# Kernel optimization log

Measured on AMD Instinct MI355X. Metric: run time of the kernel, lower is better.

## Reference

```python
import jax, jax.numpy as jnp
import numpy as np

N_NODES = 100000
N_EDGES = 1600000
N_FEAT = 128
HIDDEN = 128
N_CLASSES = 40
MAX_DEPTH = 4
INIT_TEMP = 1.0  # temperature (non-trainable)
N_AGGR = 3       # ['mean', 'max', 'self']


def setup_inputs() -> dict:
    key = jax.random.key(0)
    ks = jax.random.split(key, 16)
    s = 1.0 / np.sqrt(HIDDEN)
    inp = {
        'x': jax.random.normal(ks[0], (N_NODES, N_FEAT), dtype=jnp.float32),
        'edge_index': jax.random.randint(ks[1], (2, N_EDGES), 0, N_NODES, dtype=jnp.int32),
        'W_pre': jax.random.normal(ks[2], (N_FEAT, HIDDEN), dtype=jnp.float32) / np.sqrt(N_FEAT),
        'b_pre': jnp.zeros((HIDDEN,), dtype=jnp.float32),
        'W_depth': jax.random.normal(ks[3], (HIDDEN, 2), dtype=jnp.float32) * s,
        'b_depth': jnp.zeros((2,), dtype=jnp.float32),
        'W_aggr': jax.random.normal(ks[4], (HIDDEN, N_AGGR), dtype=jnp.float32) * s,
        'b_aggr': jnp.zeros((N_AGGR,), dtype=jnp.float32),
        'W_conv': jax.random.normal(ks[5], (MAX_DEPTH, HIDDEN, HIDDEN), dtype=jnp.float32) * s,
        'b_conv': jnp.zeros((MAX_DEPTH, HIDDEN), dtype=jnp.float32),
        'W_post': jax.random.normal(ks[6], (HIDDEN, N_CLASSES), dtype=jnp.float32) * s,
        'b_post': jnp.zeros((N_CLASSES,), dtype=jnp.float32),
    }
    return inp


def _mix_aggr_conv(x, src, dst, deg, W, b, aggr_w):
    # MixAggrConvLayer: transform then per-node convex mix of {mean, max, self}
    h = x @ W + b                                   # [N, H]
    msg = h[src]                                    # [E, H] gather
    mean_a = jax.ops.segment_sum(msg, dst, num_segments=N_NODES) / deg[:, None]
    max_a = jax.ops.segment_max(msg, dst, num_segments=N_NODES)
    max_a = jnp.where(jnp.isfinite(max_a), max_a, 0.0)  # isolated nodes -> 0
    return aggr_w[:, 0:1] * mean_a + aggr_w[:, 1:2] * max_a + aggr_w[:, 2:3] * h


def reference(x, edge_index, W_pre, b_pre, W_depth, b_depth, W_aggr, b_aggr,
              W_conv, b_conv, W_post, b_post):
    src, dst = edge_index[0], edge_index[1]
    deg = jnp.maximum(
        jax.ops.segment_sum(jnp.ones((src.shape[0],), jnp.float32), dst,
                            num_segments=N_NODES), 1.0)

    # pre_mp + (Dropout eval = identity) + ReLU
    h = jax.nn.relu(x @ W_pre + b_pre)              # [N, H]

    continue_pr = jnp.ones((N_NODES,), jnp.float32)
    selected = jnp.zeros((N_NODES, HIDDEN), jnp.float32)
    for i in range(MAX_DEPTH):
        hd = jax.lax.stop_gradient(h)               # controllers see detached x
        stop_prob = jax.nn.softmax((hd @ W_depth + b_depth) / INIT_TEMP, axis=-1)
        aggr_prob = jax.nn.softmax((hd @ W_aggr + b_aggr) / INIT_TEMP, axis=-1)
        h = _mix_aggr_conv(h, src, dst, deg, W_conv[i], b_conv[i], aggr_prob)
        h = jax.nn.relu(h)                          # dropout (eval) + relu
        selected = selected + (continue_pr * stop_prob[:, 1])[:, None] * h
        continue_pr = continue_pr * stop_prob[:, 0]

    logits = selected @ W_post + b_post             # [N, C]
    return jax.nn.log_softmax(logits, axis=1)
```

## Files before the change

kernel.cpp:

```cpp
#include <hip/hip_runtime.h>
#include <math.h>

#define HIDDEN 128
#define NCLS 40
#define BMAX 1024

typedef __attribute__((ext_vector_type(8))) short short8;
typedef __attribute__((ext_vector_type(4))) float f32x4;
typedef __attribute__((ext_vector_type(2))) float f32x2;

__device__ __forceinline__ unsigned short f2bf(float f) {
    unsigned u = __float_as_uint(f);
    unsigned r = u + 0x7FFFu + ((u >> 16) & 1u);
    return (unsigned short)(r >> 16);
}
__device__ __forceinline__ float bf_lo(unsigned u) { return __uint_as_float(u << 16); }
__device__ __forceinline__ float bf_hi(unsigned u) { return __uint_as_float(u & 0xFFFF0000u); }

__global__ void k_wprep(const float* __restrict__ Wp, const float* __restrict__ Wc,
                        const float* __restrict__ Wd, const float* __restrict__ Wa,
                        unsigned short* __restrict__ WpreT, unsigned short* __restrict__ WT) {
    int i = blockIdx.x * 256 + threadIdx.x;
    if (i < 16384) {
        int n = i >> 7, k = i & 127;
        WpreT[i] = f2bf(Wp[k * 128 + n]);
    } else if (i < 16384 + 4 * 18432) {
        int j = i - 16384;
        int d = j / 18432;
        int rem = j % 18432;
        int n = rem >> 7, k = rem & 127;
        float v = 0.f;
        if (n < 128)      v = Wc[d * 16384 + k * 128 + n];
        else if (n < 130) v = Wd[k * 2 + (n - 128)];
        else if (n < 133) v = Wa[k * 3 + (n - 130)];
        WT[j] = f2bf(v);
    }
}


__launch_bounds__(256)
__global__ void k_bcount(const int* __restrict__ ei, int E, int* __restrict__ bucket_cnt) {
    __shared__ int hist[BMAX];
    const int tid = threadIdx.x;
    for (int i = tid; i < BMAX; i += 256) hist[i] = 0;
    __syncthreads();
    const int e0 = blockIdx.x * 4096;
    #pragma unroll
    for (int i = 0; i < 16; i++) {
        int e = e0 + i * 256 + tid;
        if (e < E) atomicAdd(&hist[ei[E + e] >> 8], 1);
    }
    __syncthreads();
    for (int i = tid; i < BMAX; i += 256) {
        int v = hist[i];
        if (v > 0) atomicAdd(&bucket_cnt[i], v);
    }
}

__global__ void k_bscan(const int* __restrict__ bucket_cnt, int nb,
                        int* __restrict__ bucket_base, int* __restrict__ bucket_cursor) {
    __shared__ int sd[256];
    const int tid = threadIdx.x;
    int v[4];
    int sum = 0;
    #pragma unroll
    for (int j = 0; j < 4; j++) {
        int b = tid * 4 + j;
        v[j] = (b < nb) ? bucket_cnt[b] : 0;
        sum += v[j];
    }
    sd[tid] = sum;
    __syncthreads();
    #pragma unroll
    for (int off = 1; off < 256; off <<= 1) {
        int t = (tid >= off) ? sd[tid - off] : 0;
        __syncthreads();
        sd[tid] += t;
        __syncthreads();
    }
    int base = sd[tid] - sum;
    #pragma unroll
    for (int j = 0; j < 4; j++) {
        int b = tid * 4 + j;
        if (b < nb) {
            bucket_base[b] = base;
            bucket_cursor[b] = base;
            base += v[j];
        }
    }
}

__launch_bounds__(256)
__global__ void k_bin(const int* __restrict__ ei, int E,
                      int* __restrict__ bucket_cursor, unsigned* __restrict__ binned) {
    __shared__ int hist[BMAX];
    __shared__ int rankc[BMAX];
    __shared__ int lbase[BMAX];
    const int tid = threadIdx.x;
    const int e0 = blockIdx.x * 4096;
    for (int i = tid; i < BMAX; i += 256) { hist[i] = 0; rankc[i] = 0; }
    __syncthreads();
    int bkt[16];
    unsigned pk[16];
    #pragma unroll
    for (int i = 0; i < 16; i++) {
        int e = e0 + i * 256 + tid;
        if (e < E) {
            int s = ei[e];
            int d = ei[E + e];
            bkt[i] = d >> 8;
            pk[i] = ((unsigned)(d & 255) << 24) | (unsigned)s;
            atomicAdd(&hist[bkt[i]], 1);
        } else bkt[i] = -1;
    }
    __syncthreads();
    for (int i = tid; i < BMAX; i += 256)
        if (hist[i] > 0) lbase[i] = atomicAdd(&bucket_cursor[i], hist[i]);
    __syncthreads();
    #pragma unroll
    for (int i = 0; i < 16; i++) {
        if (bkt[i] >= 0) {
            int r = atomicAdd(&rankc[bkt[i]], 1);
            binned[lbase[bkt[i]] + r] = pk[i];
        }
    }
}

__launch_bounds__(256)
__global__ void k_scatter(const unsigned* __restrict__ binned,
                          const int* __restrict__ bucket_base,
                          const int* __restrict__ bucket_cnt,
                          int* __restrict__ row_start, int* __restrict__ deg_i,
                          float* __restrict__ degf,
                          int* __restrict__ csr_off, int N) {
    __shared__ int hist[256];
    __shared__ int rs[256];
    __shared__ int cur[256];
    const int tid = threadIdx.x;
    hist[tid] = 0;
    __syncthreads();
    const int base = bucket_base[blockIdx.x];
    const int cnt = bucket_cnt[blockIdx.x];
    for (int i = tid; i < cnt; i += 256)
        atomicAdd(&hist[binned[base + i] >> 24], 1);
    __syncthreads();
    int v = hist[tid];
    rs[tid] = v;
    __syncthreads();
    #pragma unroll
    for (int off = 1; off < 256; off <<= 1) {
        int t = (tid >= off) ? rs[tid - off] : 0;
        __syncthreads();
        rs[tid] += t;
        __syncthreads();
    }
    int gstart = base + rs[tid] - v;
    int n = (blockIdx.x << 8) + tid;
    if (n < N) {
        row_start[n] = gstart;
        deg_i[n] = v;
        degf[n] = fmaxf((float)v, 1.0f);
    }
    __syncthreads();
    rs[tid] = gstart;
    cur[tid] = 0;
    __syncthreads();
    for (int i = tid; i < cnt; i += 256) {
        unsigned p = binned[base + i];
        int dl = (int)(p >> 24);
        int r = atomicAdd(&cur[dl], 1);
        csr_off[rs[dl] + r] = (int)((p & 0xFFFFFFu) << 7);
    }
}


template <bool AF32, bool CTRL>
__launch_bounds__(256)
__global__ void k_gemm_mfma(const void* __restrict__ Ain,
                            const unsigned short* __restrict__ Wt,
                            const float* __restrict__ bias,
                            unsigned short* __restrict__ Cb,
                            unsigned char* __restrict__ C8,
                            float* __restrict__ ctrl,
                            int M, int do_relu) {
    __shared__ unsigned short Ws[144 * 132];
    const int tid = threadIdx.x;
    const int lane = tid & 63;
    const int wv = tid >> 6;
    const int row_blk = blockIdx.x * 128;
    const int rows0 = wv * 32;
    const int l15 = lane & 15;
    const int q = lane >> 4;
    const int RWS = CTRL ? 144 : 128;

    for (int c = tid; c < RWS * 16; c += 256) {
        int r = c >> 4, ch = c & 15;
        *(uint4*)&Ws[r * 132 + ch * 8] = *(const uint4*)(Wt + (size_t)r * HIDDEN + ch * 8);
    }
    __syncthreads();

    f32x4 acc[2][8] = {};
    f32x4 acc5[2] = {};
    for (int k0 = 0; k0 < 128; k0 += 32) {
        short8 af[2];
        #pragma unroll
        for (int mi = 0; mi < 2; mi++) {
            int ar = row_blk + rows0 + mi * 16 + l15;
            if (AF32) {
                const float* A = (const float*)Ain;
                float4 v0 = make_float4(0.f, 0.f, 0.f, 0.f);
                float4 v1 = make_float4(0.f, 0.f, 0.f, 0.f);
                if (ar < M) {
                    v0 = *(const float4*)(A + (size_t)ar * HIDDEN + k0 + q * 8);
                    v1 = *(const float4*)(A + (size_t)ar * HIDDEN + k0 + q * 8 + 4);
                }
                short8 t;
                t[0] = (short)f2bf(v0.x); t[1] = (short)f2bf(v0.y);
                t[2] = (short)f2bf(v0.z); t[3] = (short)f2bf(v0.w);
                t[4] = (short)f2bf(v1.x); t[5] = (short)f2bf(v1.y);
                t[6] = (short)f2bf(v1.z); t[7] = (short)f2bf(v1.w);
                af[mi] = t;
            } else {
                const unsigned short* A = (const unsigned short*)Ain;
                short8 t = {};
                if (ar < M) t = *(const short8*)(A + (size_t)ar * HIDDEN + k0 + q * 8);
                af[mi] = t;
            }
        }
        #pragma unroll
        for (int ni = 0; ni < 8; ni++) {
            short8 bw = *(const short8*)&Ws[(ni * 16 + l15) * 132 + k0 + q * 8];
            #pragma unroll
            for (int mi = 0; mi < 2; mi++)
                acc[mi][ni] = __builtin_amdgcn_mfma_f32_16x16x32_bf16(
                    bw, af[mi], acc[mi][ni], 0, 0, 0);
        }
        if (CTRL) {
            short8 bc = *(const short8*)&Ws[(128 + l15) * 132 + k0 + q * 8];
            #pragma unroll
            for (int mi = 0; mi < 2; mi++)
                acc5[mi] = __builtin_amdgcn_mfma_f32_16x16x32_bf16(
                    bc, af[mi], acc5[mi], 0, 0, 0);
        }
    }
    #pragma unroll
    for (int mi = 0; mi < 2; mi++) {
        int node = row_blk + rows0 + mi * 16 + l15;
        if (node < M) {
            #pragma unroll
            for (int ni = 0; ni < 8; ni++) {
                int fb = ni * 16 + q * 4;
                float4 bv = *(const float4*)&bias[fb];
                float o0 = acc[mi][ni][0] + bv.x;
                float o1 = acc[mi][ni][1] + bv.y;
                float o2 = acc[mi][ni][2] + bv.z;
                float o3 = acc[mi][ni][3] + bv.w;
                if (do_relu) {
                    o0 = fmaxf(o0, 0.f); o1 = fmaxf(o1, 0.f);
                    o2 = fmaxf(o2, 0.f); o3 = fmaxf(o3, 0.f);
                }
                unsigned plo, phi;
                asm("v_cvt_pk_bf16_f32 %0, %1, %2" : "=v"(plo) : "v"(o0), "v"(o1));
                asm("v_cvt_pk_bf16_f32 %0, %1, %2" : "=v"(phi) : "v"(o2), "v"(o3));
                uint2 ov;
                ov.x = plo; ov.y = phi;
                *(uint2*)(Cb + (size_t)node * HIDDEN + fb) = ov;
                if (CTRL) {
                    unsigned w8 = 0;
                    w8 = __builtin_amdgcn_cvt_pk_fp8_f32(o0, o1, w8, 0);
                    w8 = __builtin_amdgcn_cvt_pk_fp8_f32(o2, o3, w8, 1);
                    *(unsigned*)(C8 + (size_t)node * HIDDEN + fb) = w8;
                }
            }
            if (CTRL) {
                if (q == 0) {
                    *(float4*)(ctrl + (size_t)node * 8) =
                        make_float4(acc5[mi][0], acc5[mi][1], acc5[mi][2], acc5[mi][3]);
                } else if (q == 1) {
                    ctrl[(size_t)node * 8 + 4] = acc5[mi][0];
                }
            }
        }
    }
}


__launch_bounds__(256)
__global__ void k_depth(const unsigned char* __restrict__ ht8,
                        const unsigned short* __restrict__ ht,
                        unsigned short* __restrict__ h_out,
                        float* __restrict__ cp, float* __restrict__ wsel,
                        const float* __restrict__ ctrl,
                        const int* __restrict__ deg_i,
                        const int* __restrict__ row_start, const int* __restrict__ csr_off,
                        const float* __restrict__ bd, const float* __restrict__ ba,
                        int N, int first) {
    const int lane = threadIdx.x & 63;
    const int wave = threadIdx.x >> 6;
    const int node = blockIdx.x * 4 + wave;
    if (node >= N) return;
    const int nodeu = __builtin_amdgcn_readfirstlane(node);
    const int lane2 = lane << 1;

    const int cnt = deg_i[nodeu];
    const int start = row_start[nodeu];

    int soff = (lane < cnt) ? csr_off[start + lane] : 0;
    unsigned su = *(const unsigned*)((const char*)ht + ((size_t)nodeu << 8) + (lane << 2));
    float4 c4 = *(const float4*)(ctrl + (size_t)nodeu * 8);
    float cl4 = ctrl[(size_t)nodeu * 8 + 4];

    float d0 = c4.x + bd[0], d1 = c4.y + bd[1];
    float a0 = c4.z + ba[0], a1 = c4.w + ba[1], a2 = cl4 + ba[2];
    float m2 = fmaxf(d0, d1);
    float e0 = __expf(d0 - m2), e1 = __expf(d1 - m2);
    float inv2 = __builtin_amdgcn_rcpf(e0 + e1);
    float sp0 = e0 * inv2, sp1 = e1 * inv2;
    float m3 = fmaxf(fmaxf(a0, a1), a2);
    float f0 = __expf(a0 - m3), f1 = __expf(a1 - m3), f2 = __expf(a2 - m3);
    float inv3 = __builtin_amdgcn_rcpf(f0 + f1 + f2);
    float ap0 = f0 * inv3, ap1 = f1 * inv3, ap2 = f2 * inv3;

    f32x2 sacc = {0.f, 0.f};
    float mx0 = -3.4e38f, mx1 = -3.4e38f;

    #define EDGE(JJ)                                                          \
    {                                                                         \
        int so_ = __builtin_amdgcn_readlane(soff, (JJ));                      \
        const unsigned char* bp_ = ht8 + (unsigned)so_;                       \
        unsigned u_ = *(const unsigned short*)(bp_ + lane2);                  \
        f32x2 p_ = __builtin_amdgcn_cvt_pk_f32_fp8(u_, 0);                    \
        sacc += p_;                                                           \
        mx0 = fmaxf(mx0, p_.x); mx1 = fmaxf(mx1, p_.y);                       \
    }

    for (int eb = 0; eb < cnt; eb += 64) {
        if (eb) {
            int idx = eb + lane;
            soff = (idx < cnt) ? csr_off[start + idx] : 0;
        }
        int lim = min(64, cnt - eb);
        int j = 0;
        for (; j + 16 <= lim; j += 16) {
            EDGE(j)      EDGE(j + 1)  EDGE(j + 2)  EDGE(j + 3)
            EDGE(j + 4)  EDGE(j + 5)  EDGE(j + 6)  EDGE(j + 7)
            EDGE(j + 8)  EDGE(j + 9)  EDGE(j + 10) EDGE(j + 11)
            EDGE(j + 12) EDGE(j + 13) EDGE(j + 14) EDGE(j + 15)
        }
        for (; j + 4 <= lim; j += 4) {
            EDGE(j) EDGE(j + 1) EDGE(j + 2) EDGE(j + 3)
        }
        for (; j < lim; j++) EDGE(j)
    }
    #undef EDGE

    if (cnt == 0) { mx0 = 0.f; mx1 = 0.f; }
    float invd = __builtin_amdgcn_rcpf(fmaxf((float)cnt, 1.0f));
    float h0 = ap0 * (sacc.x * invd) + ap1 * mx0 + ap2 * bf_lo(su);
    float h1 = ap0 * (sacc.y * invd) + ap1 * mx1 + ap2 * bf_hi(su);
    h0 = fmaxf(h0, 0.f);
    h1 = fmaxf(h1, 0.f);
    unsigned po = ((unsigned)f2bf(h1) << 16) | (unsigned)f2bf(h0);
    *(unsigned*)((char*)h_out + ((size_t)nodeu << 8) + (lane << 2)) = po;

    if (lane == 0) {
        float cpv = first ? 1.0f : cp[nodeu];
        wsel[nodeu] = cpv * sp1;
        cp[nodeu] = cpv * sp0;
    }
}


__launch_bounds__(256)
__global__ void k_post(const unsigned short* __restrict__ h_all, size_t hstride,
                       const float* __restrict__ wsel, int N,
                       const float* __restrict__ Wp, const float* __restrict__ bp,
                       float* __restrict__ out) {
    __shared__ float Ss[32][132];
    __shared__ float Wt[NCLS][132];
    __shared__ float bs[NCLS];
    const int tid = threadIdx.x;
    const int n0 = blockIdx.x * 32;

    for (int i = tid; i < (HIDDEN * NCLS) / 4; i += 256) {
        float4 v = *(const float4*)&Wp[i * 4];
        int f = i * 4;
        int k = f / NCLS, c = f % NCLS;
        float e[4] = {v.x, v.y, v.z, v.w};
        #pragma unroll
        for (int j = 0; j < 4; j++) {
            int cc = c + j, kk = k;
            if (cc >= NCLS) { cc -= NCLS; kk++; }
            Wt[cc][kk] = e[j];
        }
    }
    if (tid < NCLS) bs[tid] = bp[tid];

    const int node_l = tid >> 3;
    const int kc = (tid & 7) * 16;
    const int ng = n0 + node_l;
    float sel[16];
    #pragma unroll
    for (int i = 0; i < 16; i++) sel[i] = 0.f;
    if (ng < N) {
        #pragma unroll
        for (int d = 0; d < 4; d++) {
            float w = wsel[(size_t)d * N + ng];
            const unsigned short* hrow = h_all + (size_t)(d + 1) * hstride + (size_t)ng * HIDDEN;
            #pragma unroll
            for (int u = 0; u < 2; u++) {
                uint4 p = *(const uint4*)(hrow + kc + u * 8);
                unsigned vs[4] = {p.x, p.y, p.z, p.w};
                #pragma unroll
                for (int j = 0; j < 4; j++) {
                    sel[u * 8 + j * 2 + 0] += w * bf_lo(vs[j]);
                    sel[u * 8 + j * 2 + 1] += w * bf_hi(vs[j]);
                }
            }
        }
    }
    #pragma unroll
    for (int u = 0; u < 4; u++)
        *(float4*)&Ss[node_l][kc + u * 4] =
            make_float4(sel[u * 4], sel[u * 4 + 1], sel[u * 4 + 2], sel[u * 4 + 3]);
    __syncthreads();

    const int c0 = (tid & 7) * 5;
    float z[5];
    #pragma unroll
    for (int i = 0; i < 5; i++) z[i] = bs[c0 + i];
    for (int k = 0; k < HIDDEN; k += 4) {
        float4 s4 = *(const float4*)&Ss[node_l][k];
        #pragma unroll
        for (int i = 0; i < 5; i++) {
            float4 w4 = *(const float4*)&Wt[c0 + i][k];
            z[i] += s4.x * w4.x + s4.y * w4.y + s4.z * w4.z + s4.w * w4.w;
        }
    }
    float m = z[0];
    #pragma unroll
    for (int i = 1; i < 5; i++) m = fmaxf(m, z[i]);
    #pragma unroll
    for (int off = 1; off < 8; off <<= 1) m = fmaxf(m, __shfl_xor(m, off));
    float s = 0.f;
    #pragma unroll
    for (int i = 0; i < 5; i++) s += expf(z[i] - m);
    #pragma unroll
    for (int off = 1; off < 8; off <<= 1) s += __shfl_xor(s, off);
    float lg = m + logf(s);
    if (ng < N) {
        #pragma unroll
        for (int i = 0; i < 5; i++)
            out[(size_t)ng * NCLS + c0 + i] = z[i] - lg;
    }
}


extern "C" void kernel_launch(void* const* d_in, const int* in_sizes, int n_in,
                              void* d_out, int out_size, void* d_ws, size_t ws_size,
                              hipStream_t stream) {
    const float* x      = (const float*)d_in[0];
    const int*   ei     = (const int*)d_in[1];
    const float* W_pre  = (const float*)d_in[2];
    const float* b_pre  = (const float*)d_in[3];
    const float* W_dep  = (const float*)d_in[4];
    const float* b_dep  = (const float*)d_in[5];
    const float* W_aggr = (const float*)d_in[6];
    const float* b_aggr = (const float*)d_in[7];
    const float* W_conv = (const float*)d_in[8];
    const float* b_conv = (const float*)d_in[9];
    const float* W_post = (const float*)d_in[10];
    const float* b_post = (const float*)d_in[11];

    const int N = in_sizes[0] / HIDDEN;
    const int E = in_sizes[1] / 2;
    const int nbuckets = (N + 255) >> 8;

    char* ws = (char*)d_ws;
    size_t off = 0;
    auto alloc = [&](size_t bytes) -> void* {
        void* p = ws + off;
        off += (bytes + 255) & ~(size_t)255;
        return p;
    };
    const size_t hstride = (size_t)N * HIDDEN;
    unsigned short* h_all  = (unsigned short*)alloc(5 * hstride * 2);
    unsigned short* ht     = (unsigned short*)alloc(hstride * 2);
    unsigned char*  ht8    = (unsigned char*)alloc(hstride);
    float* cp       = (float*)alloc((size_t)N * 4);
    float* wsel     = (float*)alloc((size_t)4 * N * 4);
    float* degf     = (float*)alloc((size_t)N * 4);
    float* ctrl     = (float*)alloc((size_t)N * 8 * 4);
    unsigned short* WpreT = (unsigned short*)alloc(128 * 128 * 2);
    unsigned short* WT    = (unsigned short*)alloc(4 * 144 * 128 * 2);
    int*   deg_i    = (int*)alloc((size_t)N * 4);
    int*   row_start= (int*)alloc((size_t)N * 4);
    int*   bucket_cnt    = (int*)alloc(BMAX * 4);
    int*   bucket_base   = (int*)alloc(BMAX * 4);
    int*   bucket_cursor = (int*)alloc(BMAX * 4);
    int*   csr_off  = (int*)alloc((size_t)E * 4);
    unsigned* binned = (unsigned*)alloc((size_t)E * 4);

    hipMemsetAsync(bucket_cnt, 0, BMAX * 4, stream);

    int ebb = (E + 4095) / 4096;
    k_bcount<<<ebb, 256, 0, stream>>>(ei, E, bucket_cnt);
    k_bscan<<<1, 256, 0, stream>>>(bucket_cnt, nbuckets, bucket_base, bucket_cursor);
    k_bin<<<ebb, 256, 0, stream>>>(ei, E, bucket_cursor, binned);
    k_scatter<<<nbuckets, 256, 0, stream>>>(binned, bucket_base, bucket_cnt,
                                            row_start, deg_i, degf, csr_off, N);

    int wtot = 16384 + 4 * 18432;
    k_wprep<<<(wtot + 255) / 256, 256, 0, stream>>>(W_pre, W_conv, W_dep, W_aggr,
                                                    WpreT, WT);

    int gblk = (N + 127) / 128;
    k_gemm_mfma<true, false><<<gblk, 256, 0, stream>>>(x, WpreT, b_pre, h_all,
                                                       nullptr, nullptr, N, 1);

    int nb4 = (N + 3) / 4;
    for (int d = 0; d < 4; d++) {
        unsigned short* h_d  = h_all + (size_t)d * hstride;
        unsigned short* h_n  = h_all + (size_t)(d + 1) * hstride;
        k_gemm_mfma<false, true><<<gblk, 256, 0, stream>>>(h_d, WT + (size_t)d * 18432,
                                                           b_conv + (size_t)d * HIDDEN,
                                                           ht, ht8, ctrl, N, 0);
        k_depth<<<nb4, 256, 0, stream>>>(ht8, ht, h_n, cp, wsel + (size_t)d * N, ctrl,
                                         deg_i, row_start, csr_off,
                                         b_dep, b_aggr, N, d == 0 ? 1 : 0);
    }
    k_post<<<(N + 31) / 32, 256, 0, stream>>>(h_all, hstride, wsel, N,
                                              W_post, b_post, (float*)d_out);
}
```

Measured before the change: 531.6 us.

## Sort nodes by degree so aggregation waves in a block get balanced work

Adds a counting sort of nodes by in-degree (histogram in the scatter kernel, a scan, then a permutation kernel) and has the per-depth aggregation kernel process nodes in that degree-sorted order. The aim is to group waves of similar edge counts into the same block so no block waits on one long wave. It costs two extra small kernels once and an extra indirection per wave. Nodes in a block are no longer contiguous, so locality of the per-node reads and writes drops. It also removes the unused float degree output.

```diff
diff --git a/kernel.cpp b/kernel.cpp
--- a/kernel.cpp
+++ b/kernel.cpp
@@ -131,13 +131,14 @@
                           const int* __restrict__ bucket_base,
                           const int* __restrict__ bucket_cnt,
                           int* __restrict__ row_start, int* __restrict__ deg_i,
-                          float* __restrict__ degf,
-                          int* __restrict__ csr_off, int N) {
+                          int* __restrict__ csr_off, int* __restrict__ dbin_cnt, int N) {
     __shared__ int hist[256];
     __shared__ int rs[256];
     __shared__ int cur[256];
+    __shared__ int dh[256];
     const int tid = threadIdx.x;
     hist[tid] = 0;
+    dh[tid] = 0;
     __syncthreads();
     const int base = bucket_base[blockIdx.x];
     const int cnt = bucket_cnt[blockIdx.x];
@@ -159,17 +160,51 @@
     if (n < N) {
         row_start[n] = gstart;
         deg_i[n] = v;
-        degf[n] = fmaxf((float)v, 1.0f);
+        atomicAdd(&dh[v < 255 ? v : 255], 1);
     }
     __syncthreads();
     rs[tid] = gstart;
     cur[tid] = 0;
+    if (dh[tid] > 0) atomicAdd(&dbin_cnt[tid], dh[tid]);
     __syncthreads();
     for (int i = tid; i < cnt; i += 256) {
         unsigned p = binned[base + i];
         int dl = (int)(p >> 24);
         int r = atomicAdd(&cur[dl], 1);
         csr_off[rs[dl] + r] = (int)((p & 0xFFFFFFu) << 7);
+    }
+}
+
+__launch_bounds__(256)
+__global__ void k_dperm(const int* __restrict__ deg_i, int N,
+                        int* __restrict__ cursor, int* __restrict__ perm) {
+    __shared__ int hist[256];
+    __shared__ int rankc[256];
+    __shared__ int lbase[256];
+    const int tid = threadIdx.x;
+    const int n0 = blockIdx.x * 1024;
+    hist[tid] = 0;
+    rankc[tid] = 0;
+    __syncthreads();
+    int dg[4];
+    #pragma unroll
+    for (int i = 0; i < 4; i++) {
+        int n = n0 + i * 256 + tid;
+        if (n < N) {
+            int d = deg_i[n];
+            dg[i] = d < 255 ? d : 255;
+            atomicAdd(&hist[dg[i]], 1);
+        } else dg[i] = -1;
+    }
+    __syncthreads();
+    if (hist[tid] > 0) lbase[tid] = atomicAdd(&cursor[tid], hist[tid]);
+    __syncthreads();
+    #pragma unroll
+    for (int i = 0; i < 4; i++) {
+        if (dg[i] >= 0) {
+            int r = atomicAdd(&rankc[dg[i]], 1);
+            perm[lbase[dg[i]] + r] = n0 + i * 256 + tid;
+        }
     }
 }
 
@@ -293,13 +328,14 @@
                         const float* __restrict__ ctrl,
                         const int* __restrict__ deg_i,
                         const int* __restrict__ row_start, const int* __restrict__ csr_off,
+                        const int* __restrict__ perm,
                         const float* __restrict__ bd, const float* __restrict__ ba,
                         int N, int first) {
     const int lane = threadIdx.x & 63;
     const int wave = threadIdx.x >> 6;
-    const int node = blockIdx.x * 4 + wave;
-    if (node >= N) return;
-    const int nodeu = __builtin_amdgcn_readfirstlane(node);
+    const int idx = blockIdx.x * 4 + wave;
+    if (idx >= N) return;
+    const int nodeu = __builtin_amdgcn_readfirstlane(perm[idx]);
     const int lane2 = lane << 1;
 
     const int cnt = deg_i[nodeu];
@@ -336,8 +372,8 @@
 
     for (int eb = 0; eb < cnt; eb += 64) {
         if (eb) {
-            int idx = eb + lane;
-            soff = (idx < cnt) ? csr_off[start + idx] : 0;
+            int i2 = eb + lane;
+            soff = (i2 < cnt) ? csr_off[start + i2] : 0;
         }
         int lim = min(64, cnt - eb);
         int j = 0;
@@ -489,26 +525,32 @@
     unsigned char*  ht8    = (unsigned char*)alloc(hstride);
     float* cp       = (float*)alloc((size_t)N * 4);
     float* wsel     = (float*)alloc((size_t)4 * N * 4);
-    float* degf     = (float*)alloc((size_t)N * 4);
     float* ctrl     = (float*)alloc((size_t)N * 8 * 4);
     unsigned short* WpreT = (unsigned short*)alloc(128 * 128 * 2);
     unsigned short* WT    = (unsigned short*)alloc(4 * 144 * 128 * 2);
     int*   deg_i    = (int*)alloc((size_t)N * 4);
     int*   row_start= (int*)alloc((size_t)N * 4);
+    int*   perm     = (int*)alloc((size_t)N * 4);
     int*   bucket_cnt    = (int*)alloc(BMAX * 4);
     int*   bucket_base   = (int*)alloc(BMAX * 4);
     int*   bucket_cursor = (int*)alloc(BMAX * 4);
+    int*   dbin_cnt      = (int*)alloc(256 * 4);
+    int*   dbin_base     = (int*)alloc(256 * 4);
+    int*   dbin_cursor   = (int*)alloc(256 * 4);
     int*   csr_off  = (int*)alloc((size_t)E * 4);
     unsigned* binned = (unsigned*)alloc((size_t)E * 4);
 
     hipMemsetAsync(bucket_cnt, 0, BMAX * 4, stream);
+    hipMemsetAsync(dbin_cnt, 0, 256 * 4, stream);
 
     int ebb = (E + 4095) / 4096;
     k_bcount<<<ebb, 256, 0, stream>>>(ei, E, bucket_cnt);
     k_bscan<<<1, 256, 0, stream>>>(bucket_cnt, nbuckets, bucket_base, bucket_cursor);
     k_bin<<<ebb, 256, 0, stream>>>(ei, E, bucket_cursor, binned);
     k_scatter<<<nbuckets, 256, 0, stream>>>(binned, bucket_base, bucket_cnt,
-                                            row_start, deg_i, degf, csr_off, N);
+                                            row_start, deg_i, csr_off, dbin_cnt, N);
+    k_bscan<<<1, 256, 0, stream>>>(dbin_cnt, 256, dbin_base, dbin_cursor);
+    k_dperm<<<(N + 1023) / 1024, 256, 0, stream>>>(deg_i, N, dbin_cursor, perm);
 
     int wtot = 16384 + 4 * 18432;
     k_wprep<<<(wtot + 255) / 256, 256, 0, stream>>>(W_pre, W_conv, W_dep, W_aggr,
@@ -526,7 +568,7 @@
                                                            b_conv + (size_t)d * HIDDEN,
                                                            ht, ht8, ctrl, N, 0);
         k_depth<<<nb4, 256, 0, stream>>>(ht8, ht, h_n, cp, wsel + (size_t)d * N, ctrl,
-                                         deg_i, row_start, csr_off,
+                                         deg_i, row_start, csr_off, perm,
                                          b_dep, b_aggr, N, d == 0 ? 1 : 0);
     }
     k_post<<<(N + 31) / 32, 256, 0, stream>>>(h_all, hstride, wsel, N,
```

Result: slower. 558.3 us (+5.0%).
